# Kernel tuning notes

Hardware: AMD Instinct MI355X
Metric: run time of the kernel (lower is better)

Reference implementation:

```python
import jax, jax.numpy as jnp
import numpy as np

B, S, D = 2, 2048, 1024
QKV = 2048
H = 16
HD = QKV // H  # 128
SCALE = HD ** -0.5


def setup_inputs() -> dict:
    key = jax.random.key(0)
    k1, k2, k3, k4, k5 = jax.random.split(key, 5)
    std = D ** -0.5
    return {
        "x": jax.random.normal(k1, (B, S, D), dtype=jnp.float32),
        "wq": jax.random.normal(k2, (QKV, D), dtype=jnp.float32) * std,
        "wk": jax.random.normal(k3, (QKV, D), dtype=jnp.float32) * std,
        "wv": jax.random.normal(k4, (QKV, D), dtype=jnp.float32) * std,
        "wo": jax.random.normal(k5, (D, QKV), dtype=jnp.float32) * (QKV ** -0.5),
    }


def reference(x, wq, wk, wv, wo):
    b, s, _ = x.shape
    # QKV projections (torch Linear: y = x @ W.T), reshape to [b, h, s, hd]
    q = (x @ wq.T).reshape(b, s, H, HD).transpose(0, 2, 1, 3)
    k = (x @ wk.T).reshape(b, s, H, HD).transpose(0, 2, 1, 3)
    v = (x @ wv.T).reshape(b, s, H, HD).transpose(0, 2, 1, 3)
    scores = jnp.einsum("bhqd,bhkd->bhqk", q, k) * SCALE
    causal = jnp.tril(jnp.ones((s, s), dtype=bool))
    scores = jnp.where(causal[None, None], scores, -jnp.inf)
    attn = jax.nn.softmax(scores, axis=-1)  # dropout p=0 (eval)
    out = jnp.einsum("bhqk,bhkd->bhqd", attn, v)
    out = out.transpose(0, 2, 1, 3).reshape(b, s, QKV)
    return out @ wo.T
```

## Files before the change

### kernel.cpp

```cpp
#include <hip/hip_runtime.h>
#include <hip/hip_bf16.h>
#include <cstdint>

#define SEQ   2048
#define DMOD  1024
#define QKVD  2048
#define NH    16
#define HDIM  128
#define NTOK  4096

typedef __bf16 bf16;
typedef bf16 bf16x4 __attribute__((ext_vector_type(4)));
typedef bf16 bf16x8 __attribute__((ext_vector_type(8)));
typedef float f32x4 __attribute__((ext_vector_type(4)));
typedef float f32x16 __attribute__((ext_vector_type(16)));
typedef uint32_t u32x4 __attribute__((ext_vector_type(4)));

typedef __attribute__((address_space(1))) void* as1_t;
typedef __attribute__((address_space(3))) void* as3_t;

__device__ __forceinline__ void gload16(const void* g, void* l) {
  __builtin_amdgcn_global_load_lds((as1_t)(uintptr_t)g, (as3_t)(uintptr_t)l, 16, 0, 0);
}

__device__ __forceinline__ uint32_t pkbf(float a, float b) {
  union { bf16 h; unsigned short u; } x, y;
  x.h = (bf16)a; y.h = (bf16)b;
  return (uint32_t)x.u | ((uint32_t)y.u << 16);
}

__device__ __forceinline__ void plswap(uint32_t& a, uint32_t& b) {
  asm("v_permlane32_swap_b32 %0, %1" : "+v"(a), "+v"(b));
}

__global__ void cast_f32_bf16(const float* __restrict__ in, bf16* __restrict__ out, int n4) {
  int i = blockIdx.x * blockDim.x + threadIdx.x;
  if (i < n4) {
    float4 v = reinterpret_cast<const float4*>(in)[i];
    bf16x4 o;
    o[0] = (bf16)v.x; o[1] = (bf16)v.y; o[2] = (bf16)v.z; o[3] = (bf16)v.w;
    reinterpret_cast<bf16x4*>(out)[i] = o;
  }
}

__global__ void cast_w4(const float* __restrict__ p0, const float* __restrict__ p1,
                        const float* __restrict__ p2, const float* __restrict__ p3,
                        bf16* __restrict__ out) {
  int i = blockIdx.x * blockDim.x + threadIdx.x;
  const float* src = (i < 524288) ? p0 : (i < 1048576) ? p1 : (i < 1572864) ? p2 : p3;
  int off = i & 524287;
  float4 v = reinterpret_cast<const float4*>(src)[off];
  bf16x4 o;
  o[0] = (bf16)v.x; o[1] = (bf16)v.y; o[2] = (bf16)v.z; o[3] = (bf16)v.w;
  reinterpret_cast<bf16x4*>(out)[i] = o;
}

__global__ __launch_bounds__(512, 1) void qkv_gemm_kernel(
    const bf16* __restrict__ A, const bf16* __restrict__ Bw,
    bf16* __restrict__ Qo, bf16* __restrict__ Ko, bf16* __restrict__ Vto, float qs)
{
  __shared__ bf16 RING[3][24576];

  const int tid  = threadIdx.x;
  const int lane = tid & 63;
  const int wid  = tid >> 6;
  const int wm   = wid >> 2;
  const int wn   = wid & 3;
  const int lm   = lane & 15;
  const int lg   = lane >> 4;

  const int g   = blockIdx.x & 7;
  const int idx = blockIdx.x >> 3;
  const int m0  = ((g & 1) * 16 + (idx & 15)) * 128;
  const int n0  = ((g >> 1) * 6 + (idx >> 4)) * 256;

  f32x4 acc[4][4];
#pragma unroll
  for (int i = 0; i < 4; ++i)
#pragma unroll
    for (int j = 0; j < 4; ++j) acc[i][j] = (f32x4)0.0f;

  const int rl = lane >> 3;
  const int cbb = (lane & 7) * 16;

  auto stageA = [&](int kt, int slot) {
    const int k0 = kt * 64;
    char* Ab = (char*)&RING[slot][0];
#pragma unroll
    for (int r2 = 0; r2 < 2; ++r2) {
      int chunk = r2 * 8 + wid;
      int row   = chunk * 8 + rl;
      int cx    = cbb ^ ((row & 7) << 4);
      gload16(A + (size_t)(m0 + row) * DMOD + k0 + (cx >> 1), Ab + chunk * 1024);
    }
  };
  auto stageB1 = [&](int kt, int slot, int r2) {
    const int k0 = kt * 64;
    char* Bb = (char*)&RING[slot][0] + 16384;
    int chunk = r2 * 8 + wid;
    int row   = chunk * 8 + rl;
    int cx    = cbb ^ ((row & 7) << 4);
    gload16(Bw + (size_t)(n0 + row) * DMOD + k0 + (cx >> 1), Bb + chunk * 1024);
  };
  auto stageFull = [&](int kt, int slot) {
    stageA(kt, slot);
#pragma unroll
    for (int r2 = 0; r2 < 4; ++r2) stageB1(kt, slot, r2);
  };

  auto rdA = [&](const char* Ab, int mf, int kk) -> bf16x8 {
    int row = wm * 64 + mf * 16 + lm;
    int cx  = (kk * 64 + lg * 16) ^ ((row & 7) << 4);
    return *(const bf16x8*)(Ab + row * 128 + cx);
  };
  auto rdB = [&](const char* Bb, int nf, int kk) -> bf16x8 {
    int row = wn * 64 + nf * 16 + lm;
    int cx  = (kk * 64 + lg * 16) ^ ((row & 7) << 4);
    return *(const bf16x8*)(Bb + row * 128 + cx);
  };

  stageFull(0, 0);
  stageFull(1, 1);

  int cur = 0;
  for (int t = 0; t < 16; ++t) {
    if (t < 15) asm volatile("s_waitcnt vmcnt(6)" ::: "memory");
    else        asm volatile("s_waitcnt vmcnt(0)" ::: "memory");
    __builtin_amdgcn_s_barrier();

    const char* Ab = (const char*)&RING[cur][0];
    const char* Bb = Ab + 16384;
    const bool pf = (t + 2 < 16);
    const int  ps = (cur + 2 >= 3) ? (cur - 1) : (cur + 2);

    bf16x8 a[4], b[2];

#pragma unroll
    for (int mf = 0; mf < 4; ++mf) a[mf] = rdA(Ab, mf, 0);
    b[0] = rdB(Bb, 0, 0); b[1] = rdB(Bb, 1, 0);
    if (pf) stageA(t + 2, ps);
    __builtin_amdgcn_s_barrier();
    asm volatile("s_waitcnt lgkmcnt(0)" ::: "memory");
    __builtin_amdgcn_s_setprio(1);
#pragma unroll
    for (int mf = 0; mf < 4; ++mf) {
      acc[mf][0] = __builtin_amdgcn_mfma_f32_16x16x32_bf16(a[mf], b[0], acc[mf][0], 0, 0, 0);
      acc[mf][1] = __builtin_amdgcn_mfma_f32_16x16x32_bf16(a[mf], b[1], acc[mf][1], 0, 0, 0);
    }
    __builtin_amdgcn_s_setprio(0);
    __builtin_amdgcn_s_barrier();

    b[0] = rdB(Bb, 2, 0); b[1] = rdB(Bb, 3, 0);
    if (pf) { stageB1(t + 2, ps, 0); stageB1(t + 2, ps, 1); }
    __builtin_amdgcn_s_barrier();
    asm volatile("s_waitcnt lgkmcnt(0)" ::: "memory");
    __builtin_amdgcn_s_setprio(1);
#pragma unroll
    for (int mf = 0; mf < 4; ++mf) {
      acc[mf][2] = __builtin_amdgcn_mfma_f32_16x16x32_bf16(a[mf], b[0], acc[mf][2], 0, 0, 0);
      acc[mf][3] = __builtin_amdgcn_mfma_f32_16x16x32_bf16(a[mf], b[1], acc[mf][3], 0, 0, 0);
    }
    __builtin_amdgcn_s_setprio(0);
    __builtin_amdgcn_s_barrier();

#pragma unroll
    for (int mf = 0; mf < 4; ++mf) a[mf] = rdA(Ab, mf, 1);
    b[0] = rdB(Bb, 0, 1); b[1] = rdB(Bb, 1, 1);
    if (pf) stageB1(t + 2, ps, 2);
    __builtin_amdgcn_s_barrier();
    asm volatile("s_waitcnt lgkmcnt(0)" ::: "memory");
    __builtin_amdgcn_s_setprio(1);
#pragma unroll
    for (int mf = 0; mf < 4; ++mf) {
      acc[mf][0] = __builtin_amdgcn_mfma_f32_16x16x32_bf16(a[mf], b[0], acc[mf][0], 0, 0, 0);
      acc[mf][1] = __builtin_amdgcn_mfma_f32_16x16x32_bf16(a[mf], b[1], acc[mf][1], 0, 0, 0);
    }
    __builtin_amdgcn_s_setprio(0);
    __builtin_amdgcn_s_barrier();

    b[0] = rdB(Bb, 2, 1); b[1] = rdB(Bb, 3, 1);
    if (pf) stageB1(t + 2, ps, 3);
    __builtin_amdgcn_s_barrier();
    asm volatile("s_waitcnt lgkmcnt(0)" ::: "memory");
    __builtin_amdgcn_s_setprio(1);
#pragma unroll
    for (int mf = 0; mf < 4; ++mf) {
      acc[mf][2] = __builtin_amdgcn_mfma_f32_16x16x32_bf16(a[mf], b[0], acc[mf][2], 0, 0, 0);
      acc[mf][3] = __builtin_amdgcn_mfma_f32_16x16x32_bf16(a[mf], b[1], acc[mf][3], 0, 0, 0);
    }
    __builtin_amdgcn_s_setprio(0);
    __builtin_amdgcn_s_barrier();

    cur = (cur == 2) ? 0 : cur + 1;
  }

#pragma unroll
  for (int mf = 0; mf < 4; ++mf) {
#pragma unroll
    for (int nf = 0; nf < 4; ++nf) {
      int row0 = m0 + wm * 64 + mf * 16 + lg * 4;
      int col  = n0 + wn * 64 + nf * 16 + lm;
      f32x4 cv = acc[mf][nf];
      if (n0 < 2048) {
#pragma unroll
        for (int r = 0; r < 4; ++r)
          Qo[(size_t)(row0 + r) * QKVD + col] = (bf16)(cv[r] * qs);
      } else if (n0 < 4096) {
        int kc = col - 2048;
#pragma unroll
        for (int r = 0; r < 4; ++r)
          Ko[(size_t)(row0 + r) * QKVD + kc] = (bf16)cv[r];
      } else {
        int vc = col - 4096;
#pragma unroll
        for (int r = 0; r < 4; ++r) {
          int tok = row0 + r; int bb = tok >> 11; int s = tok & 2047;
          Vto[((size_t)bb * QKVD + vc) * SEQ + s] = (bf16)cv[r];
        }
      }
    }
  }
}

__global__ __launch_bounds__(256, 2) void proj_kernel(
    const bf16* __restrict__ A, const bf16* __restrict__ Bw, float* __restrict__ out)
{
  __shared__ bf16 RING[2][16384];

  const int tid  = threadIdx.x;
  const int lane = tid & 63;
  const int wid  = tid >> 6;
  const int wm   = wid >> 1;
  const int wn   = wid & 1;
  const int lm   = lane & 15;
  const int lg   = lane >> 4;

  const int g   = blockIdx.x & 7;
  const int idx = blockIdx.x >> 3;
  const int m0  = (g * 4 + (idx >> 3)) * 128;
  const int n0  = (idx & 7) * 128;

  f32x4 acc[4][4];
#pragma unroll
  for (int i = 0; i < 4; ++i)
#pragma unroll
    for (int j = 0; j < 4; ++j) acc[i][j] = (f32x4)0.0f;

  const int rl = lane >> 3;
  const int cbb = (lane & 7) * 16;

  auto stage = [&](int kt, int slot) {
    const int k0 = kt * 64;
    char* Ab = (char*)&RING[slot][0];
    char* Bb = Ab + 16384;
#pragma unroll
    for (int r2 = 0; r2 < 4; ++r2) {
      int chunk = r2 * 4 + wid;
      int row   = chunk * 8 + rl;
      int cx    = cbb ^ ((row & 7) << 4);
      gload16(A + (size_t)(m0 + row) * QKVD + k0 + (cx >> 1), Ab + chunk * 1024);
    }
#pragma unroll
    for (int r2 = 0; r2 < 4; ++r2) {
      int chunk = r2 * 4 + wid;
      int row   = chunk * 8 + rl;
      int cx    = cbb ^ ((row & 7) << 4);
      gload16(Bw + (size_t)(n0 + row) * QKVD + k0 + (cx >> 1), Bb + chunk * 1024);
    }
  };

  auto rdA = [&](const char* Ab, int mf, int kk) -> bf16x8 {
    int row = wm * 64 + mf * 16 + lm;
    int cx  = (kk * 64 + lg * 16) ^ ((row & 7) << 4);
    return *(const bf16x8*)(Ab + row * 128 + cx);
  };
  auto rdB = [&](const char* Bb, int nf, int kk) -> bf16x8 {
    int row = wn * 64 + nf * 16 + lm;
    int cx  = (kk * 64 + lg * 16) ^ ((row & 7) << 4);
    return *(const bf16x8*)(Bb + row * 128 + cx);
  };

  stage(0, 0);

  int cur = 0;
  for (int t = 0; t < 32; ++t) {
    if (t < 31) {
      stage(t + 1, cur ^ 1);
      asm volatile("s_waitcnt vmcnt(8)" ::: "memory");
    } else {
      asm volatile("s_waitcnt vmcnt(0)" ::: "memory");
    }
    __builtin_amdgcn_s_barrier();

    const char* Ab = (const char*)&RING[cur][0];
    const char* Bb = Ab + 16384;

    bf16x8 a[4], b[2];

#pragma unroll
    for (int mf = 0; mf < 4; ++mf) a[mf] = rdA(Ab, mf, 0);
    b[0] = rdB(Bb, 0, 0); b[1] = rdB(Bb, 1, 0);
    __builtin_amdgcn_s_barrier();
    asm volatile("s_waitcnt lgkmcnt(0)" ::: "memory");
    __builtin_amdgcn_s_setprio(1);
#pragma unroll
    for (int mf = 0; mf < 4; ++mf) {
      acc[mf][0] = __builtin_amdgcn_mfma_f32_16x16x32_bf16(a[mf], b[0], acc[mf][0], 0, 0, 0);
      acc[mf][1] = __builtin_amdgcn_mfma_f32_16x16x32_bf16(a[mf], b[1], acc[mf][1], 0, 0, 0);
    }
    __builtin_amdgcn_s_setprio(0);
    __builtin_amdgcn_s_barrier();

    b[0] = rdB(Bb, 2, 0); b[1] = rdB(Bb, 3, 0);
    __builtin_amdgcn_s_barrier();
    asm volatile("s_waitcnt lgkmcnt(0)" ::: "memory");
    __builtin_amdgcn_s_setprio(1);
#pragma unroll
    for (int mf = 0; mf < 4; ++mf) {
      acc[mf][2] = __builtin_amdgcn_mfma_f32_16x16x32_bf16(a[mf], b[0], acc[mf][2], 0, 0, 0);
      acc[mf][3] = __builtin_amdgcn_mfma_f32_16x16x32_bf16(a[mf], b[1], acc[mf][3], 0, 0, 0);
    }
    __builtin_amdgcn_s_setprio(0);
    __builtin_amdgcn_s_barrier();

#pragma unroll
    for (int mf = 0; mf < 4; ++mf) a[mf] = rdA(Ab, mf, 1);
    b[0] = rdB(Bb, 0, 1); b[1] = rdB(Bb, 1, 1);
    __builtin_amdgcn_s_barrier();
    asm volatile("s_waitcnt lgkmcnt(0)" ::: "memory");
    __builtin_amdgcn_s_setprio(1);
#pragma unroll
    for (int mf = 0; mf < 4; ++mf) {
      acc[mf][0] = __builtin_amdgcn_mfma_f32_16x16x32_bf16(a[mf], b[0], acc[mf][0], 0, 0, 0);
      acc[mf][1] = __builtin_amdgcn_mfma_f32_16x16x32_bf16(a[mf], b[1], acc[mf][1], 0, 0, 0);
    }
    __builtin_amdgcn_s_setprio(0);
    __builtin_amdgcn_s_barrier();

    b[0] = rdB(Bb, 2, 1); b[1] = rdB(Bb, 3, 1);
    __builtin_amdgcn_s_barrier();
    asm volatile("s_waitcnt lgkmcnt(0)" ::: "memory");
    __builtin_amdgcn_s_setprio(1);
#pragma unroll
    for (int mf = 0; mf < 4; ++mf) {
      acc[mf][2] = __builtin_amdgcn_mfma_f32_16x16x32_bf16(a[mf], b[0], acc[mf][2], 0, 0, 0);
      acc[mf][3] = __builtin_amdgcn_mfma_f32_16x16x32_bf16(a[mf], b[1], acc[mf][3], 0, 0, 0);
    }
    __builtin_amdgcn_s_setprio(0);
    __builtin_amdgcn_s_barrier();

    cur ^= 1;
  }

#pragma unroll
  for (int mf = 0; mf < 4; ++mf)
#pragma unroll
    for (int nf = 0; nf < 4; ++nf) {
      int row0 = m0 + wm * 64 + mf * 16 + lg * 4;
      int col  = n0 + wn * 64 + nf * 16 + lm;
      f32x4 cv = acc[mf][nf];
#pragma unroll
      for (int r = 0; r < 4; ++r)
        out[(size_t)(row0 + r) * DMOD + col] = cv[r];
    }
}

__global__ __launch_bounds__(256, 2) void flash_kernel(
    const bf16* __restrict__ Q, const bf16* __restrict__ Kg,
    const bf16* __restrict__ Vt, bf16* __restrict__ Po, float2* __restrict__ Pml)
{
  __shared__ bf16 KV[2][16384];

  const int tid  = threadIdx.x;
  const int lane = tid & 63;
  const int wid  = tid >> 6;
  const int l31  = lane & 31;
  const int lh   = lane >> 5;

  const int id   = blockIdx.x;
  const int bh   = (id & 7) * 4 + ((id >> 3) & 3);
  const int xx   = id >> 5;
  const int pr   = xx >> 1;
  const int qpar = xx & 1;
  const int b    = bh >> 4;
  const int h    = bh & 15;

  auto stage = [&](int j, int buf) {
    bf16* kb = &KV[buf][0];
    bf16* vb = &KV[buf][8192];
    const int rb0 = wid * 16;
#pragma unroll
    for (int i = 0; i < 4; ++i) {
      int r0 = rb0 + i * 4;
      int r  = r0 + (lane >> 4);
      int c  = ((lane & 15) * 16) ^ ((r & 15) << 4);
      gload16(Kg + ((size_t)(b * SEQ + j * 64 + r)) * QKVD + h * HDIM + (c >> 1),
              kb + r0 * 128);
    }
    const int db0 = wid * 32;
#pragma unroll
    for (int i = 0; i < 4; ++i) {
      int d0 = db0 + i * 8;
      int d  = d0 + (lane >> 3);
      int c  = ((lane & 7) * 16) ^ ((d & 7) << 4);
      gload16(Vt + ((size_t)(bh * HDIM + d)) * SEQ + j * 64 + (c >> 1),
              vb + d0 * 64);
    }
  };

  for (int sub = 0; sub < 2; ++sub) {
    const int T  = sub ? (15 - pr) : pr;
    const int nu = T + 1;
    const int rA = T * 128 + wid * 32;

    bf16x8 qfr[8];
    {
      const bf16* qb = Q + ((size_t)(b * SEQ + rA + l31)) * QKVD + h * HDIM + lh * 8;
#pragma unroll
      for (int st = 0; st < 8; ++st) qfr[st] = *reinterpret_cast<const bf16x8*>(qb + st * 16);
    }

    f32x16 o[4];
#pragma unroll
    for (int c = 0; c < 4; ++c) o[c] = (f32x16)0.0f;
    float mreg = -__builtin_inff();
    float lreg = 0.0f;

    stage(qpar, 0);
    __syncthreads();

    int cur = 0;
    for (int i = 0; i < nu; ++i) {
      const int j = qpar + 2 * i;
      if (i + 1 < nu) stage(qpar + 2 * (i + 1), cur ^ 1);

      const bool act = (j * 64 <= rA + 31);
      if (act) {
        const char* kbb = (const char*)&KV[cur][0];
        const char* vbb = kbb + 16384;

        f32x16 s0 = (f32x16)0.0f, s1 = (f32x16)0.0f;
#pragma unroll
        for (int st = 0; st < 8; ++st) {
          const int r0 = l31, r1 = 32 + l31;
          bf16x8 kf0 = *(const bf16x8*)(kbb + r0 * 256 + ((lh * 16 + st * 32) ^ ((r0 & 15) << 4)));
          bf16x8 kf1 = *(const bf16x8*)(kbb + r1 * 256 + ((lh * 16 + st * 32) ^ ((r1 & 15) << 4)));
          s0 = __builtin_amdgcn_mfma_f32_32x32x16_bf16(kf0, qfr[st], s0, 0, 0, 0);
          s1 = __builtin_amdgcn_mfma_f32_32x32x16_bf16(kf1, qfr[st], s1, 0, 0, 0);
        }

        const bool full = (j * 64 + 63) <= rA;
        if (!full) {
          const int qr  = rA + l31;
          const int kb0 = j * 64 + 4 * lh;
#pragma unroll
          for (int r = 0; r < 16; ++r) {
            int key = kb0 + (r & 3) + 8 * (r >> 2);
            if (key > qr)      s0[r] = -1e30f;
            if (key + 32 > qr) s1[r] = -1e30f;
          }
        }

        float mx = s0[0];
#pragma unroll
        for (int r = 1; r < 16; ++r) mx = fmaxf(mx, s0[r]);
#pragma unroll
        for (int r = 0; r < 16; ++r) mx = fmaxf(mx, s1[r]);
        mx = fmaxf(mx, __shfl_xor(mx, 32));

        float mn;
        if (__all(mx <= mreg + 8.0f)) {
          mn = mreg;
        } else {
          mn = fmaxf(mreg, mx);
          float scl = exp2f(mreg - mn);
          mreg = mn;
          lreg *= scl;
#pragma unroll
          for (int r = 0; r < 16; ++r) {
            int row = (r & 3) + 8 * (r >> 2) + 4 * lh;
            float sr = __shfl(scl, row);
#pragma unroll
            for (int c = 0; c < 4; ++c) o[c][r] *= sr;
          }
        }

        float p[32];
#pragma unroll
        for (int r = 0; r < 16; ++r) p[r]      = exp2f(s0[r] - mn);
#pragma unroll
        for (int r = 0; r < 16; ++r) p[16 + r] = exp2f(s1[r] - mn);
        float rs = 0.0f;
#pragma unroll
        for (int r = 0; r < 32; ++r) rs += p[r];
        rs += __shfl_xor(rs, 32);
        lreg += rs;

        bf16x8 pa[4];
#pragma unroll
        for (int f = 0; f < 4; ++f) {
          const float* pp = p + f * 8;
          uint32_t w0 = pkbf(pp[0], pp[1]);
          uint32_t w1 = pkbf(pp[2], pp[3]);
          uint32_t w2 = pkbf(pp[4], pp[5]);
          uint32_t w3 = pkbf(pp[6], pp[7]);
          plswap(w0, w2);
          plswap(w1, w3);
          u32x4 w = {w0, w1, w2, w3};
          pa[f] = __builtin_bit_cast(bf16x8, w);
        }

#pragma unroll
        for (int c = 0; c < 4; ++c) {
          const int d = c * 32 + l31;
          const char* vrow = vbb + d * 128;
          const int dx = (d & 7) << 4;
#pragma unroll
          for (int f = 0; f < 4; ++f) {
            bf16x8 vf = *(const bf16x8*)(vrow + ((f * 32 + lh * 16) ^ dx));
            o[c] = __builtin_amdgcn_mfma_f32_32x32x16_bf16(pa[f], vf, o[c], 0, 0, 0);
          }
        }
      }

      __syncthreads();
      cur ^= 1;
    }

    const int part = (bh * 16 + T) * 2 + qpar;
#pragma unroll
    for (int c = 0; c < 4; ++c)
#pragma unroll
      for (int r = 0; r < 16; ++r) {
        int row = (r & 3) + 8 * (r >> 2) + 4 * lh;
        Po[((size_t)part * 128 + wid * 32 + row) * 128 + c * 32 + l31] = (bf16)o[c][r];
      }
    if (lane < 32)
      Pml[part * 128 + wid * 32 + lane] = make_float2(mreg, lreg);
  }
}

__global__ void merge_kernel(const bf16* __restrict__ Po, const float2* __restrict__ Pml,
                             bf16* __restrict__ Ob)
{
  const int id  = blockIdx.x;
  const int bh  = id >> 4;
  const int t   = id & 15;
  const int tid = threadIdx.x;
  const int row = tid >> 1;
  const int dh  = (tid & 1) * 64;
  const int p0  = id * 2, p1 = id * 2 + 1;

  float2 ml0 = Pml[p0 * 128 + row];
  float2 ml1 = Pml[p1 * 128 + row];
  float M  = fmaxf(ml0.x, ml1.x);
  float w0 = exp2f(ml0.x - M);
  float w1 = exp2f(ml1.x - M);
  float inv = 1.0f / (ml0.y * w0 + ml1.y * w1);
  w0 *= inv; w1 *= inv;

  const bf16* o0 = Po + ((size_t)p0 * 128 + row) * 128 + dh;
  const bf16* o1 = Po + ((size_t)p1 * 128 + row) * 128 + dh;
  const int b = bh >> 4, h = bh & 15;
  bf16* out = Ob + ((size_t)(b * SEQ + t * 128 + row)) * QKVD + h * HDIM + dh;

#pragma unroll
  for (int v = 0; v < 8; ++v) {
    bf16x8 a = reinterpret_cast<const bf16x8*>(o0)[v];
    bf16x8 c = reinterpret_cast<const bf16x8*>(o1)[v];
    bf16x8 w;
#pragma unroll
    for (int k = 0; k < 8; ++k) w[k] = (bf16)((float)a[k] * w0 + (float)c[k] * w1);
    reinterpret_cast<bf16x8*>(out)[v] = w;
  }
}

extern "C" void kernel_launch(void* const* d_in, const int* in_sizes, int n_in,
                              void* d_out, int out_size, void* d_ws, size_t ws_size,
                              hipStream_t stream) {
  const float* x  = (const float*)d_in[0];
  const float* wq = (const float*)d_in[1];
  const float* wk = (const float*)d_in[2];
  const float* wv = (const float*)d_in[3];
  const float* wo = (const float*)d_in[4];
  float* out = (float*)d_out;

  bf16* xb  = (bf16*)d_ws;
  bf16* wqb = xb  + (size_t)NTOK * DMOD;
  bf16* wob = wqb + (size_t)3 * QKVD * DMOD;
  bf16* Qb  = wob + (size_t)DMOD * QKVD;
  bf16* Kb  = Qb  + (size_t)NTOK * QKVD;
  bf16* Vtb = Kb  + (size_t)NTOK * QKVD;
  bf16* Ob  = Vtb + (size_t)NTOK * QKVD;
  bf16* Po  = Ob  + (size_t)NTOK * QKVD;
  float2* Pml = (float2*)(Po + (size_t)1024 * 128 * 128);

  cast_f32_bf16<<<(NTOK * DMOD / 4) / 256, 256, 0, stream>>>(x, xb, NTOK * DMOD / 4);
  cast_w4<<<8192, 256, 0, stream>>>(wq, wk, wv, wo, wqb);

  const float qs = 0.08838834764831845f * 1.4426950408889634f;
  qkv_gemm_kernel<<<768, 512, 0, stream>>>(xb, wqb, Qb, Kb, Vtb, qs);

  flash_kernel<<<512, 256, 0, stream>>>(Qb, Kb, Vtb, Po, Pml);
  merge_kernel<<<512, 256, 0, stream>>>(Po, Pml, Ob);

  proj_kernel<<<256, 256, 0, stream>>>(Ob, wob, out);
}
```

Measured before the change: 190.6 us.

## Enlarge QKV GEMM tile to 256x256 with 32x32 MFMA and double buffering

The QKV projection GEMM now uses 256x256 output tiles instead of 128x256, halving the grid to 384 blocks. Each wave computes a 128x64 sub-tile with 32x32x16 bf16 MFMA instructions and f32x16 accumulators. The 3-slot ring with split staging becomes a 2-buffer scheme that waits for all loads each iteration. The aim is more operand reuse per LDS read and fewer global loads. The cost is less prefetch depth, a full vmcnt(0) stall per k-step, and only 384 blocks to spread across the CUs.

```diff
diff --git a/kernel.cpp b/kernel.cpp
--- a/kernel.cpp
+++ b/kernel.cpp
@@ -59,163 +59,121 @@
     const bf16* __restrict__ A, const bf16* __restrict__ Bw,
     bf16* __restrict__ Qo, bf16* __restrict__ Ko, bf16* __restrict__ Vto, float qs)
 {
-  __shared__ bf16 RING[3][24576];
+  __shared__ bf16 BUF[2][32768];
 
   const int tid  = threadIdx.x;
   const int lane = tid & 63;
   const int wid  = tid >> 6;
   const int wm   = wid >> 2;
   const int wn   = wid & 3;
-  const int lm   = lane & 15;
-  const int lg   = lane >> 4;
+  const int l31  = lane & 31;
+  const int lh   = lane >> 5;
 
   const int g   = blockIdx.x & 7;
   const int idx = blockIdx.x >> 3;
-  const int m0  = ((g & 1) * 16 + (idx & 15)) * 128;
-  const int n0  = ((g >> 1) * 6 + (idx >> 4)) * 256;
-
-  f32x4 acc[4][4];
+  const int m0  = ((g & 1) * 8 + (idx & 7)) * 256;
+  const int n0  = ((g >> 1) * 6 + (idx >> 3)) * 256;
+
+  f32x16 acc[4][2];
 #pragma unroll
   for (int i = 0; i < 4; ++i)
 #pragma unroll
-    for (int j = 0; j < 4; ++j) acc[i][j] = (f32x4)0.0f;
-
-  const int rl = lane >> 3;
+    for (int j = 0; j < 2; ++j) acc[i][j] = (f32x16)0.0f;
+
+  const int rl  = lane >> 3;
   const int cbb = (lane & 7) * 16;
 
-  auto stageA = [&](int kt, int slot) {
+  auto stage = [&](int kt, int buf) {
     const int k0 = kt * 64;
-    char* Ab = (char*)&RING[slot][0];
-#pragma unroll
-    for (int r2 = 0; r2 < 2; ++r2) {
+    char* Ab = (char*)&BUF[buf][0];
+    char* Bb = Ab + 32768;
+#pragma unroll
+    for (int r2 = 0; r2 < 4; ++r2) {
       int chunk = r2 * 8 + wid;
       int row   = chunk * 8 + rl;
       int cx    = cbb ^ ((row & 7) << 4);
       gload16(A + (size_t)(m0 + row) * DMOD + k0 + (cx >> 1), Ab + chunk * 1024);
     }
-  };
-  auto stageB1 = [&](int kt, int slot, int r2) {
-    const int k0 = kt * 64;
-    char* Bb = (char*)&RING[slot][0] + 16384;
-    int chunk = r2 * 8 + wid;
-    int row   = chunk * 8 + rl;
-    int cx    = cbb ^ ((row & 7) << 4);
-    gload16(Bw + (size_t)(n0 + row) * DMOD + k0 + (cx >> 1), Bb + chunk * 1024);
-  };
-  auto stageFull = [&](int kt, int slot) {
-    stageA(kt, slot);
-#pragma unroll
-    for (int r2 = 0; r2 < 4; ++r2) stageB1(kt, slot, r2);
-  };
-
-  auto rdA = [&](const char* Ab, int mf, int kk) -> bf16x8 {
-    int row = wm * 64 + mf * 16 + lm;
-    int cx  = (kk * 64 + lg * 16) ^ ((row & 7) << 4);
+#pragma unroll
+    for (int r2 = 0; r2 < 4; ++r2) {
+      int chunk = r2 * 8 + wid;
+      int row   = chunk * 8 + rl;
+      int cx    = cbb ^ ((row & 7) << 4);
+      gload16(Bw + (size_t)(n0 + row) * DMOD + k0 + (cx >> 1), Bb + chunk * 1024);
+    }
+  };
+
+  auto rdA = [&](const char* Ab, int mf, int ks) -> bf16x8 {
+    int row = wm * 128 + mf * 32 + l31;
+    int cx  = (ks * 32 + lh * 16) ^ ((row & 7) << 4);
     return *(const bf16x8*)(Ab + row * 128 + cx);
   };
-  auto rdB = [&](const char* Bb, int nf, int kk) -> bf16x8 {
-    int row = wn * 64 + nf * 16 + lm;
-    int cx  = (kk * 64 + lg * 16) ^ ((row & 7) << 4);
+  auto rdB = [&](const char* Bb, int nf, int ks) -> bf16x8 {
+    int row = wn * 64 + nf * 32 + l31;
+    int cx  = (ks * 32 + lh * 16) ^ ((row & 7) << 4);
     return *(const bf16x8*)(Bb + row * 128 + cx);
   };
 
-  stageFull(0, 0);
-  stageFull(1, 1);
-
-  int cur = 0;
+  stage(0, 0);
+
   for (int t = 0; t < 16; ++t) {
-    if (t < 15) asm volatile("s_waitcnt vmcnt(6)" ::: "memory");
-    else        asm volatile("s_waitcnt vmcnt(0)" ::: "memory");
-    __builtin_amdgcn_s_barrier();
-
-    const char* Ab = (const char*)&RING[cur][0];
-    const char* Bb = Ab + 16384;
-    const bool pf = (t + 2 < 16);
-    const int  ps = (cur + 2 >= 3) ? (cur - 1) : (cur + 2);
-
-    bf16x8 a[4], b[2];
-
-#pragma unroll
-    for (int mf = 0; mf < 4; ++mf) a[mf] = rdA(Ab, mf, 0);
-    b[0] = rdB(Bb, 0, 0); b[1] = rdB(Bb, 1, 0);
-    if (pf) stageA(t + 2, ps);
-    __builtin_amdgcn_s_barrier();
-    asm volatile("s_waitcnt lgkmcnt(0)" ::: "memory");
-    __builtin_amdgcn_s_setprio(1);
-#pragma unroll
-    for (int mf = 0; mf < 4; ++mf) {
-      acc[mf][0] = __builtin_amdgcn_mfma_f32_16x16x32_bf16(a[mf], b[0], acc[mf][0], 0, 0, 0);
-      acc[mf][1] = __builtin_amdgcn_mfma_f32_16x16x32_bf16(a[mf], b[1], acc[mf][1], 0, 0, 0);
-    }
-    __builtin_amdgcn_s_setprio(0);
-    __builtin_amdgcn_s_barrier();
-
-    b[0] = rdB(Bb, 2, 0); b[1] = rdB(Bb, 3, 0);
-    if (pf) { stageB1(t + 2, ps, 0); stageB1(t + 2, ps, 1); }
-    __builtin_amdgcn_s_barrier();
-    asm volatile("s_waitcnt lgkmcnt(0)" ::: "memory");
-    __builtin_amdgcn_s_setprio(1);
-#pragma unroll
-    for (int mf = 0; mf < 4; ++mf) {
-      acc[mf][2] = __builtin_amdgcn_mfma_f32_16x16x32_bf16(a[mf], b[0], acc[mf][2], 0, 0, 0);
-      acc[mf][3] = __builtin_amdgcn_mfma_f32_16x16x32_bf16(a[mf], b[1], acc[mf][3], 0, 0, 0);
-    }
-    __builtin_amdgcn_s_setprio(0);
-    __builtin_amdgcn_s_barrier();
-
-#pragma unroll
-    for (int mf = 0; mf < 4; ++mf) a[mf] = rdA(Ab, mf, 1);
-    b[0] = rdB(Bb, 0, 1); b[1] = rdB(Bb, 1, 1);
-    if (pf) stageB1(t + 2, ps, 2);
-    __builtin_amdgcn_s_barrier();
-    asm volatile("s_waitcnt lgkmcnt(0)" ::: "memory");
-    __builtin_amdgcn_s_setprio(1);
-#pragma unroll
-    for (int mf = 0; mf < 4; ++mf) {
-      acc[mf][0] = __builtin_amdgcn_mfma_f32_16x16x32_bf16(a[mf], b[0], acc[mf][0], 0, 0, 0);
-      acc[mf][1] = __builtin_amdgcn_mfma_f32_16x16x32_bf16(a[mf], b[1], acc[mf][1], 0, 0, 0);
-    }
-    __builtin_amdgcn_s_setprio(0);
-    __builtin_amdgcn_s_barrier();
-
-    b[0] = rdB(Bb, 2, 1); b[1] = rdB(Bb, 3, 1);
-    if (pf) stageB1(t + 2, ps, 3);
-    __builtin_amdgcn_s_barrier();
-    asm volatile("s_waitcnt lgkmcnt(0)" ::: "memory");
-    __builtin_amdgcn_s_setprio(1);
-#pragma unroll
-    for (int mf = 0; mf < 4; ++mf) {
-      acc[mf][2] = __builtin_amdgcn_mfma_f32_16x16x32_bf16(a[mf], b[0], acc[mf][2], 0, 0, 0);
-      acc[mf][3] = __builtin_amdgcn_mfma_f32_16x16x32_bf16(a[mf], b[1], acc[mf][3], 0, 0, 0);
-    }
-    __builtin_amdgcn_s_setprio(0);
-    __builtin_amdgcn_s_barrier();
-
-    cur = (cur == 2) ? 0 : cur + 1;
+    const int c = t & 1;
+    asm volatile("s_waitcnt vmcnt(0)" ::: "memory");
+    __builtin_amdgcn_s_barrier();
+    if (t < 15) stage(t + 1, c ^ 1);
+
+    const char* Ab = (const char*)&BUF[c][0];
+    const char* Bb = Ab + 32768;
+
+#pragma unroll
+    for (int kp = 0; kp < 2; ++kp) {
+      bf16x8 a[4][2], b[2];
+#pragma unroll
+      for (int mf = 0; mf < 4; ++mf)
+#pragma unroll
+        for (int q = 0; q < 2; ++q) a[mf][q] = rdA(Ab, mf, kp * 2 + q);
+      b[0] = rdB(Bb, 0, kp * 2); b[1] = rdB(Bb, 0, kp * 2 + 1);
+      __builtin_amdgcn_s_barrier();
+      asm volatile("s_waitcnt lgkmcnt(0)" ::: "memory");
+      __builtin_amdgcn_s_setprio(1);
+#pragma unroll
+      for (int mf = 0; mf < 4; ++mf) {
+        acc[mf][0] = __builtin_amdgcn_mfma_f32_32x32x16_bf16(a[mf][0], b[0], acc[mf][0], 0, 0, 0);
+        acc[mf][0] = __builtin_amdgcn_mfma_f32_32x32x16_bf16(a[mf][1], b[1], acc[mf][0], 0, 0, 0);
+      }
+      __builtin_amdgcn_s_setprio(0);
+      __builtin_amdgcn_s_barrier();
+
+      b[0] = rdB(Bb, 1, kp * 2); b[1] = rdB(Bb, 1, kp * 2 + 1);
+      __builtin_amdgcn_s_barrier();
+      asm volatile("s_waitcnt lgkmcnt(0)" ::: "memory");
+      __builtin_amdgcn_s_setprio(1);
+#pragma unroll
+      for (int mf = 0; mf < 4; ++mf) {
+        acc[mf][1] = __builtin_amdgcn_mfma_f32_32x32x16_bf16(a[mf][0], b[0], acc[mf][1], 0, 0, 0);
+        acc[mf][1] = __builtin_amdgcn_mfma_f32_32x32x16_bf16(a[mf][1], b[1], acc[mf][1], 0, 0, 0);
+      }
+      __builtin_amdgcn_s_setprio(0);
+      __builtin_amdgcn_s_barrier();
+    }
   }
 
 #pragma unroll
   for (int mf = 0; mf < 4; ++mf) {
 #pragma unroll
-    for (int nf = 0; nf < 4; ++nf) {
-      int row0 = m0 + wm * 64 + mf * 16 + lg * 4;
-      int col  = n0 + wn * 64 + nf * 16 + lm;
-      f32x4 cv = acc[mf][nf];
-      if (n0 < 2048) {
-#pragma unroll
-        for (int r = 0; r < 4; ++r)
-          Qo[(size_t)(row0 + r) * QKVD + col] = (bf16)(cv[r] * qs);
-      } else if (n0 < 4096) {
-        int kc = col - 2048;
-#pragma unroll
-        for (int r = 0; r < 4; ++r)
-          Ko[(size_t)(row0 + r) * QKVD + kc] = (bf16)cv[r];
-      } else {
-        int vc = col - 4096;
-#pragma unroll
-        for (int r = 0; r < 4; ++r) {
-          int tok = row0 + r; int bb = tok >> 11; int s = tok & 2047;
-          Vto[((size_t)bb * QKVD + vc) * SEQ + s] = (bf16)cv[r];
+    for (int nf = 0; nf < 2; ++nf) {
+      f32x16 cv = acc[mf][nf];
+      int col = n0 + wn * 64 + nf * 32 + l31;
+#pragma unroll
+      for (int r = 0; r < 16; ++r) {
+        int row0 = m0 + wm * 128 + mf * 32 + (r & 3) + 8 * (r >> 2) + 4 * lh;
+        if (n0 < 2048) {
+          Qo[(size_t)row0 * QKVD + col] = (bf16)(cv[r] * qs);
+        } else if (n0 < 4096) {
+          Ko[(size_t)row0 * QKVD + (col - 2048)] = (bf16)cv[r];
+        } else {
+          int bb = row0 >> 11; int s = row0 & 2047;
+          Vto[((size_t)bb * QKVD + (col - 4096)) * SEQ + s] = (bf16)cv[r];
         }
       }
     }
@@ -599,7 +557,7 @@
   cast_w4<<<8192, 256, 0, stream>>>(wq, wk, wv, wo, wqb);
 
   const float qs = 0.08838834764831845f * 1.4426950408889634f;
-  qkv_gemm_kernel<<<768, 512, 0, stream>>>(xb, wqb, Qb, Kb, Vtb, qs);
+  qkv_gemm_kernel<<<384, 512, 0, stream>>>(xb, wqb, Qb, Kb, Vtb, qs);
 
   flash_kernel<<<512, 256, 0, stream>>>(Qb, Kb, Vtb, Po, Pml);
   merge_kernel<<<512, 256, 0, stream>>>(Po, Pml, Ob);
```

New measurement: 250.1 us. 1.31x slower.

## Drop split-KV partials and merge kernel; each block owns one full query tile

Applied to the files above, without the earlier changes.

Previously each block handled two paired query tiles (T and 15-T) but split keys by parity into two partial outputs, which a separate merge kernel then combined. Now each of the 512 blocks processes one query tile over all its key blocks, normalizes in-kernel and writes O directly. This removes the partial-output round trip through memory and one kernel launch. The cost is less even per-block load: blocks range from 2 to 32 KV iterations, paired only via the blockIdx ordering.

```diff
diff --git a/kernel.cpp b/kernel.cpp
--- a/kernel.cpp
+++ b/kernel.cpp
@@ -367,7 +367,7 @@
 
 __global__ __launch_bounds__(256, 2) void flash_kernel(
     const bf16* __restrict__ Q, const bf16* __restrict__ Kg,
-    const bf16* __restrict__ Vt, bf16* __restrict__ Po, float2* __restrict__ Pml)
+    const bf16* __restrict__ Vt, bf16* __restrict__ O)
 {
   __shared__ bf16 KV[2][16384];
 
@@ -377,13 +377,16 @@
   const int l31  = lane & 31;
   const int lh   = lane >> 5;
 
-  const int id   = blockIdx.x;
-  const int bh   = (id & 7) * 4 + ((id >> 3) & 3);
-  const int xx   = id >> 5;
-  const int pr   = xx >> 1;
-  const int qpar = xx & 1;
-  const int b    = bh >> 4;
-  const int h    = bh & 15;
+  const int id  = blockIdx.x;
+  const int c   = id & 255;
+  const int s   = id >> 8;
+  const int bh  = (c & 7) * 4 + ((c >> 3) & 3);
+  const int k   = (c >> 5) & 7;
+  const int T   = s ? (15 - k) : k;
+  const int nu  = 2 * (T + 1);
+  const int b   = bh >> 4;
+  const int h   = bh & 15;
+  const int rA  = T * 128 + wid * 32;
 
   auto stage = [&](int j, int buf) {
     bf16* kb = &KV[buf][0];
@@ -393,8 +396,8 @@
     for (int i = 0; i < 4; ++i) {
       int r0 = rb0 + i * 4;
       int r  = r0 + (lane >> 4);
-      int c  = ((lane & 15) * 16) ^ ((r & 15) << 4);
-      gload16(Kg + ((size_t)(b * SEQ + j * 64 + r)) * QKVD + h * HDIM + (c >> 1),
+      int cc = ((lane & 15) * 16) ^ ((r & 15) << 4);
+      gload16(Kg + ((size_t)(b * SEQ + j * 64 + r)) * QKVD + h * HDIM + (cc >> 1),
               kb + r0 * 128);
     }
     const int db0 = wid * 32;
@@ -402,177 +405,135 @@
     for (int i = 0; i < 4; ++i) {
       int d0 = db0 + i * 8;
       int d  = d0 + (lane >> 3);
-      int c  = ((lane & 7) * 16) ^ ((d & 7) << 4);
-      gload16(Vt + ((size_t)(bh * HDIM + d)) * SEQ + j * 64 + (c >> 1),
+      int cc = ((lane & 7) * 16) ^ ((d & 7) << 4);
+      gload16(Vt + ((size_t)(bh * HDIM + d)) * SEQ + j * 64 + (cc >> 1),
               vb + d0 * 64);
     }
   };
 
-  for (int sub = 0; sub < 2; ++sub) {
-    const int T  = sub ? (15 - pr) : pr;
-    const int nu = T + 1;
-    const int rA = T * 128 + wid * 32;
-
-    bf16x8 qfr[8];
-    {
-      const bf16* qb = Q + ((size_t)(b * SEQ + rA + l31)) * QKVD + h * HDIM + lh * 8;
-#pragma unroll
-      for (int st = 0; st < 8; ++st) qfr[st] = *reinterpret_cast<const bf16x8*>(qb + st * 16);
-    }
-
-    f32x16 o[4];
-#pragma unroll
-    for (int c = 0; c < 4; ++c) o[c] = (f32x16)0.0f;
-    float mreg = -__builtin_inff();
-    float lreg = 0.0f;
-
-    stage(qpar, 0);
-    __syncthreads();
-
-    int cur = 0;
-    for (int i = 0; i < nu; ++i) {
-      const int j = qpar + 2 * i;
-      if (i + 1 < nu) stage(qpar + 2 * (i + 1), cur ^ 1);
-
-      const bool act = (j * 64 <= rA + 31);
-      if (act) {
-        const char* kbb = (const char*)&KV[cur][0];
-        const char* vbb = kbb + 16384;
-
-        f32x16 s0 = (f32x16)0.0f, s1 = (f32x16)0.0f;
-#pragma unroll
-        for (int st = 0; st < 8; ++st) {
-          const int r0 = l31, r1 = 32 + l31;
-          bf16x8 kf0 = *(const bf16x8*)(kbb + r0 * 256 + ((lh * 16 + st * 32) ^ ((r0 & 15) << 4)));
-          bf16x8 kf1 = *(const bf16x8*)(kbb + r1 * 256 + ((lh * 16 + st * 32) ^ ((r1 & 15) << 4)));
-          s0 = __builtin_amdgcn_mfma_f32_32x32x16_bf16(kf0, qfr[st], s0, 0, 0, 0);
-          s1 = __builtin_amdgcn_mfma_f32_32x32x16_bf16(kf1, qfr[st], s1, 0, 0, 0);
-        }
-
-        const bool full = (j * 64 + 63) <= rA;
-        if (!full) {
-          const int qr  = rA + l31;
-          const int kb0 = j * 64 + 4 * lh;
-#pragma unroll
-          for (int r = 0; r < 16; ++r) {
-            int key = kb0 + (r & 3) + 8 * (r >> 2);
-            if (key > qr)      s0[r] = -1e30f;
-            if (key + 32 > qr) s1[r] = -1e30f;
-          }
-        }
-
-        float mx = s0[0];
-#pragma unroll
-        for (int r = 1; r < 16; ++r) mx = fmaxf(mx, s0[r]);
-#pragma unroll
-        for (int r = 0; r < 16; ++r) mx = fmaxf(mx, s1[r]);
-        mx = fmaxf(mx, __shfl_xor(mx, 32));
-
-        float mn;
-        if (__all(mx <= mreg + 8.0f)) {
-          mn = mreg;
-        } else {
-          mn = fmaxf(mreg, mx);
-          float scl = exp2f(mreg - mn);
-          mreg = mn;
-          lreg *= scl;
-#pragma unroll
-          for (int r = 0; r < 16; ++r) {
-            int row = (r & 3) + 8 * (r >> 2) + 4 * lh;
-            float sr = __shfl(scl, row);
-#pragma unroll
-            for (int c = 0; c < 4; ++c) o[c][r] *= sr;
-          }
-        }
-
-        float p[32];
-#pragma unroll
-        for (int r = 0; r < 16; ++r) p[r]      = exp2f(s0[r] - mn);
-#pragma unroll
-        for (int r = 0; r < 16; ++r) p[16 + r] = exp2f(s1[r] - mn);
-        float rs = 0.0f;
-#pragma unroll
-        for (int r = 0; r < 32; ++r) rs += p[r];
-        rs += __shfl_xor(rs, 32);
-        lreg += rs;
-
-        bf16x8 pa[4];
-#pragma unroll
-        for (int f = 0; f < 4; ++f) {
-          const float* pp = p + f * 8;
-          uint32_t w0 = pkbf(pp[0], pp[1]);
-          uint32_t w1 = pkbf(pp[2], pp[3]);
-          uint32_t w2 = pkbf(pp[4], pp[5]);
-          uint32_t w3 = pkbf(pp[6], pp[7]);
-          plswap(w0, w2);
-          plswap(w1, w3);
-          u32x4 w = {w0, w1, w2, w3};
-          pa[f] = __builtin_bit_cast(bf16x8, w);
-        }
-
-#pragma unroll
-        for (int c = 0; c < 4; ++c) {
-          const int d = c * 32 + l31;
-          const char* vrow = vbb + d * 128;
-          const int dx = (d & 7) << 4;
-#pragma unroll
-          for (int f = 0; f < 4; ++f) {
-            bf16x8 vf = *(const bf16x8*)(vrow + ((f * 32 + lh * 16) ^ dx));
-            o[c] = __builtin_amdgcn_mfma_f32_32x32x16_bf16(pa[f], vf, o[c], 0, 0, 0);
-          }
+  bf16x8 qfr[8];
+  {
+    const bf16* qb = Q + ((size_t)(b * SEQ + rA + l31)) * QKVD + h * HDIM + lh * 8;
+#pragma unroll
+    for (int st = 0; st < 8; ++st) qfr[st] = *reinterpret_cast<const bf16x8*>(qb + st * 16);
+  }
+
+  f32x16 o[4];
+#pragma unroll
+  for (int cc = 0; cc < 4; ++cc) o[cc] = (f32x16)0.0f;
+  float mreg = -__builtin_inff();
+  float lreg = 0.0f;
+
+  stage(0, 0);
+  __syncthreads();
+
+  int cur = 0;
+  for (int j = 0; j < nu; ++j) {
+    if (j + 1 < nu) stage(j + 1, cur ^ 1);
+
+    const bool act = (j * 64 <= rA + 31);
+    if (act) {
+      const char* kbb = (const char*)&KV[cur][0];
+      const char* vbb = kbb + 16384;
+
+      f32x16 s0 = (f32x16)0.0f, s1 = (f32x16)0.0f;
+#pragma unroll
+      for (int st = 0; st < 8; ++st) {
+        const int r0 = l31, r1 = 32 + l31;
+        bf16x8 kf0 = *(const bf16x8*)(kbb + r0 * 256 + ((lh * 16 + st * 32) ^ ((r0 & 15) << 4)));
+        bf16x8 kf1 = *(const bf16x8*)(kbb + r1 * 256 + ((lh * 16 + st * 32) ^ ((r1 & 15) << 4)));
+        s0 = __builtin_amdgcn_mfma_f32_32x32x16_bf16(kf0, qfr[st], s0, 0, 0, 0);
+        s1 = __builtin_amdgcn_mfma_f32_32x32x16_bf16(kf1, qfr[st], s1, 0, 0, 0);
+      }
+
+      const bool full = (j * 64 + 63) <= rA;
+      if (!full) {
+        const int qr  = rA + l31;
+        const int kb0 = j * 64 + 4 * lh;
+#pragma unroll
+        for (int r = 0; r < 16; ++r) {
+          int key = kb0 + (r & 3) + 8 * (r >> 2);
+          if (key > qr)      s0[r] = -1e30f;
+          if (key + 32 > qr) s1[r] = -1e30f;
         }
       }
 
-      __syncthreads();
-      cur ^= 1;
-    }
-
-    const int part = (bh * 16 + T) * 2 + qpar;
-#pragma unroll
-    for (int c = 0; c < 4; ++c)
-#pragma unroll
-      for (int r = 0; r < 16; ++r) {
-        int row = (r & 3) + 8 * (r >> 2) + 4 * lh;
-        Po[((size_t)part * 128 + wid * 32 + row) * 128 + c * 32 + l31] = (bf16)o[c][r];
+      float mx = s0[0];
+#pragma unroll
+      for (int r = 1; r < 16; ++r) mx = fmaxf(mx, s0[r]);
+#pragma unroll
+      for (int r = 0; r < 16; ++r) mx = fmaxf(mx, s1[r]);
+      mx = fmaxf(mx, __shfl_xor(mx, 32));
+
+      float mn;
+      if (__all(mx <= mreg + 8.0f)) {
+        mn = mreg;
+      } else {
+        mn = fmaxf(mreg, mx);
+        float scl = exp2f(mreg - mn);
+        mreg = mn;
+        lreg *= scl;
+#pragma unroll
+        for (int r = 0; r < 16; ++r) {
+          int row = (r & 3) + 8 * (r >> 2) + 4 * lh;
+          float sr = __shfl(scl, row);
+#pragma unroll
+          for (int cc = 0; cc < 4; ++cc) o[cc][r] *= sr;
+        }
       }
-    if (lane < 32)
-      Pml[part * 128 + wid * 32 + lane] = make_float2(mreg, lreg);
+
+      float p[32];
+#pragma unroll
+      for (int r = 0; r < 16; ++r) p[r]      = exp2f(s0[r] - mn);
+#pragma unroll
+      for (int r = 0; r < 16; ++r) p[16 + r] = exp2f(s1[r] - mn);
+      float rs = 0.0f;
+#pragma unroll
+      for (int r = 0; r < 32; ++r) rs += p[r];
+      rs += __shfl_xor(rs, 32);
+      lreg += rs;
+
+      bf16x8 pa[4];
+#pragma unroll
+      for (int f = 0; f < 4; ++f) {
+        const float* pp = p + f * 8;
+        uint32_t w0 = pkbf(pp[0], pp[1]);
+        uint32_t w1 = pkbf(pp[2], pp[3]);
+        uint32_t w2 = pkbf(pp[4], pp[5]);
+        uint32_t w3 = pkbf(pp[6], pp[7]);
+        plswap(w0, w2);
+        plswap(w1, w3);
+        u32x4 w = {w0, w1, w2, w3};
+        pa[f] = __builtin_bit_cast(bf16x8, w);
+      }
+
+#pragma unroll
+      for (int cc = 0; cc < 4; ++cc) {
+        const int d = cc * 32 + l31;
+        const char* vrow = vbb + d * 128;
+        const int dx = (d & 7) << 4;
+#pragma unroll
+        for (int f = 0; f < 4; ++f) {
+          bf16x8 vf = *(const bf16x8*)(vrow + ((f * 32 + lh * 16) ^ dx));
+          o[cc] = __builtin_amdgcn_mfma_f32_32x32x16_bf16(pa[f], vf, o[cc], 0, 0, 0);
+        }
+      }
+    }
+
+    __syncthreads();
+    cur ^= 1;
   }
-}
-
-__global__ void merge_kernel(const bf16* __restrict__ Po, const float2* __restrict__ Pml,
-                             bf16* __restrict__ Ob)
-{
-  const int id  = blockIdx.x;
-  const int bh  = id >> 4;
-  const int t   = id & 15;
-  const int tid = threadIdx.x;
-  const int row = tid >> 1;
-  const int dh  = (tid & 1) * 64;
-  const int p0  = id * 2, p1 = id * 2 + 1;
-
-  float2 ml0 = Pml[p0 * 128 + row];
-  float2 ml1 = Pml[p1 * 128 + row];
-  float M  = fmaxf(ml0.x, ml1.x);
-  float w0 = exp2f(ml0.x - M);
-  float w1 = exp2f(ml1.x - M);
-  float inv = 1.0f / (ml0.y * w0 + ml1.y * w1);
-  w0 *= inv; w1 *= inv;
-
-  const bf16* o0 = Po + ((size_t)p0 * 128 + row) * 128 + dh;
-  const bf16* o1 = Po + ((size_t)p1 * 128 + row) * 128 + dh;
-  const int b = bh >> 4, h = bh & 15;
-  bf16* out = Ob + ((size_t)(b * SEQ + t * 128 + row)) * QKVD + h * HDIM + dh;
-
-#pragma unroll
-  for (int v = 0; v < 8; ++v) {
-    bf16x8 a = reinterpret_cast<const bf16x8*>(o0)[v];
-    bf16x8 c = reinterpret_cast<const bf16x8*>(o1)[v];
-    bf16x8 w;
-#pragma unroll
-    for (int k = 0; k < 8; ++k) w[k] = (bf16)((float)a[k] * w0 + (float)c[k] * w1);
-    reinterpret_cast<bf16x8*>(out)[v] = w;
-  }
+
+  float linv = 1.0f / lreg;
+#pragma unroll
+  for (int cc = 0; cc < 4; ++cc)
+#pragma unroll
+    for (int r = 0; r < 16; ++r) {
+      int row = (r & 3) + 8 * (r >> 2) + 4 * lh;
+      float li = __shfl(linv, row);
+      O[((size_t)(b * SEQ + rA + row)) * QKVD + h * HDIM + cc * 32 + l31] =
+          (bf16)(o[cc][r] * li);
+    }
 }
 
 extern "C" void kernel_launch(void* const* d_in, const int* in_sizes, int n_in,
@@ -592,8 +553,6 @@
   bf16* Kb  = Qb  + (size_t)NTOK * QKVD;
   bf16* Vtb = Kb  + (size_t)NTOK * QKVD;
   bf16* Ob  = Vtb + (size_t)NTOK * QKVD;
-  bf16* Po  = Ob  + (size_t)NTOK * QKVD;
-  float2* Pml = (float2*)(Po + (size_t)1024 * 128 * 128);
 
   cast_f32_bf16<<<(NTOK * DMOD / 4) / 256, 256, 0, stream>>>(x, xb, NTOK * DMOD / 4);
   cast_w4<<<8192, 256, 0, stream>>>(wq, wk, wv, wo, wqb);
@@ -601,8 +560,7 @@
   const float qs = 0.08838834764831845f * 1.4426950408889634f;
   qkv_gemm_kernel<<<768, 512, 0, stream>>>(xb, wqb, Qb, Kb, Vtb, qs);
 
-  flash_kernel<<<512, 256, 0, stream>>>(Qb, Kb, Vtb, Po, Pml);
-  merge_kernel<<<512, 256, 0, stream>>>(Po, Pml, Ob);
+  flash_kernel<<<512, 256, 0, stream>>>(Qb, Kb, Vtb, Ob);
 
   proj_kernel<<<256, 256, 0, stream>>>(Ob, wob, out);
 }
```

Result: faster. 179.1 us (-6.0%).
